# Kernel optimization log

Hardware: AMD Instinct MI355X
Metric: run time of the kernel (lower is better)

The kernel has to match this reference:

```python
import jax, jax.numpy as jnp
import numpy as np

B, S, H = 8, 2048, 1024

def setup_inputs() -> dict:
    key = jax.random.key(0)
    ks = jax.random.split(key, 7)
    scale = 1.0 / np.sqrt(H)
    return {
        "x": jax.random.normal(ks[0], (B, S, H), dtype=jnp.float32),
        "Wq": jax.random.uniform(ks[1], (H, H), jnp.float32, -scale, scale),
        "bq": jax.random.uniform(ks[2], (H,), jnp.float32, -scale, scale),
        "Wk": jax.random.uniform(ks[3], (H, H), jnp.float32, -scale, scale),
        "bk": jax.random.uniform(ks[4], (H,), jnp.float32, -scale, scale),
        "Wv": jax.random.uniform(ks[5], (H, H), jnp.float32, -scale, scale),
        "bv": jax.random.uniform(ks[6], (H,), jnp.float32, -scale, scale),
    }

def reference(x, Wq, bq, Wk, bk, Wv, bv):
    # nn.Linear: x @ W.T + b  (dropout_rate=0.0 -> identity)
    q = jnp.einsum("bsh,oh->bso", x, Wq) + bq
    k = jnp.einsum("bsh,oh->bso", x, Wk) + bk
    v = jnp.einsum("bsh,oh->bso", x, Wv) + bv
    # NOTE: original module applies NO 1/sqrt(d) scaling
    scores = jnp.einsum("bqh,bkh->bqk", q, k)  # [B,S,S]
    probs = jax.nn.softmax(scores, axis=-1)
    context = jnp.einsum("bqk,bkh->bqh", probs, v)  # [B,S,H]
    return context
```

## Files before the change

### kernel.cpp

```cpp
#include <hip/hip_runtime.h>
#include <stdint.h>

typedef unsigned short UST;
typedef __attribute__((ext_vector_type(8))) short    bf16x8;
typedef __attribute__((ext_vector_type(4))) float    f32x4;
typedef __attribute__((ext_vector_type(4))) float    float4_t;
typedef __attribute__((ext_vector_type(4))) UST      ushort4_t;
typedef __attribute__((ext_vector_type(8))) UST      ushort8_t;

__device__ __forceinline__ UST f2bf(float f) {
    union { float f; uint32_t u; } c; c.f = f;
    uint32_t u = c.u;
    u = (u + 0x7FFFu + ((u >> 16) & 1u)) >> 16;
    return (UST)u;
}
__device__ __forceinline__ float bf2f(UST h) {
    union { uint32_t u; float f; } c; c.u = ((uint32_t)h) << 16;
    return c.f;
}

__device__ __forceinline__ void async_copy16(const void* g, void* l) {
    __builtin_amdgcn_global_load_lds(
        (const __attribute__((address_space(1))) uint32_t*)g,
        (__attribute__((address_space(3))) uint32_t*)l, 16, 0, 0);
}

__device__ __forceinline__ void xcd_remap(int& bx, int& by, int& bz) {
    const int gx = (int)gridDim.x, gy = (int)gridDim.y, gz = (int)gridDim.z;
    const int nwg = gx * gy * gz;
    if (nwg & 7) return;
    int flat = ((int)blockIdx.z * gy + (int)blockIdx.y) * gx + (int)blockIdx.x;
    const int q = nwg >> 3;
    int s = (flat & 7) * q + (flat >> 3);
    bx = s % gx; s /= gx;
    by = s % gy;
    bz = s / gy;
}

__global__ void split_kernel(const float* __restrict__ in, UST* __restrict__ hi,
                             UST* __restrict__ lo, int n4) {
    int i = blockIdx.x * blockDim.x + threadIdx.x;
    int stride = gridDim.x * blockDim.x;
    for (; i < n4; i += stride) {
        float4_t v = *(const float4_t*)(in + (size_t)i * 4);
        ushort4_t h, l;
#pragma unroll
        for (int j = 0; j < 4; j++) {
            float f = v[j];
            UST hh = f2bf(f);
            h[j] = hh;
            l[j] = f2bf(f - bf2f(hh));
        }
        *(ushort4_t*)(hi + (size_t)i * 4) = h;
        *(ushort4_t*)(lo + (size_t)i * 4) = l;
    }
}

__global__ void cvt_hi_kernel(const float* __restrict__ in, UST* __restrict__ hi, int n4) {
    int i = blockIdx.x * blockDim.x + threadIdx.x;
    int stride = gridDim.x * blockDim.x;
    for (; i < n4; i += stride) {
        float4_t v = *(const float4_t*)(in + (size_t)i * 4);
        ushort4_t h;
#pragma unroll
        for (int j = 0; j < 4; j++) h[j] = f2bf(v[j]);
        *(ushort4_t*)(hi + (size_t)i * 4) = h;
    }
}

template <int OUT_MODE, bool HAS_BIAS>
__global__ __launch_bounds__(512, 2)
void gemm3_256(const UST* __restrict__ Ah, const UST* __restrict__ Al,
               const UST* __restrict__ Bh, const UST* __restrict__ Bl,
               const float* __restrict__ bias,
               void* __restrict__ C0, void* __restrict__ C1,
               int K, int ldc,
               long long sA, long long sB, long long sC) {
    constexpr int TILE = 8192;
    constexpr int HALF = 4 * TILE;
    __shared__ UST lds[2 * HALF];

    int bx = (int)blockIdx.x, by = (int)blockIdx.y, bz = (int)blockIdx.z;
    xcd_remap(bx, by, bz);
    const int brow = by * 256;
    const int bcol = bx * 256;

    const int t = threadIdx.x;
    const int wave = t >> 6, lane = t & 63;
    const int wr = (wave >> 2) * 128;
    const int wc = (wave & 3) * 64;
    const int lr = lane & 15, lg = lane >> 4;

    const int srow0 = t >> 2;
    const int scol_sw = (((t & 3) ^ ((srow0 >> 1) & 3))) * 8;

    int offA[8], offB[4];
#pragma unroll
    for (int m = 0; m < 8; m++) {
        int r = wr + m * 16 + lr;
        offA[m] = r * 32 + ((lg ^ ((r >> 1) & 3)) << 3);
    }
#pragma unroll
    for (int n = 0; n < 4; n++) {
        int r = wc + n * 16 + lr;
        offB[n] = r * 32 + ((lg ^ ((r >> 1) & 3)) << 3);
    }

    f32x4 acc[8][4];
#pragma unroll
    for (int m = 0; m < 8; m++)
#pragma unroll
        for (int n = 0; n < 4; n++) acc[m][n] = (f32x4){0.f, 0.f, 0.f, 0.f};

    const UST* pAh = Ah + (long long)bz * sA;
    const UST* pAl = Al + (long long)bz * sA;
    const UST* pBh = Bh + (long long)bz * sB;
    const UST* pBl = Bl + (long long)bz * sB;

    {
        const UST* gAh = pAh + (size_t)(brow + srow0) * (size_t)K + scol_sw;
        async_copy16(gAh, lds + t * 8);
        async_copy16(gAh + (size_t)128 * K, lds + 4096 + t * 8);
        const UST* gAl = pAl + (size_t)(brow + srow0) * (size_t)K + scol_sw;
        async_copy16(gAl, lds + TILE + t * 8);
        async_copy16(gAl + (size_t)128 * K, lds + TILE + 4096 + t * 8);
        const UST* gBh = pBh + (size_t)(bcol + srow0) * (size_t)K + scol_sw;
        async_copy16(gBh, lds + 2 * TILE + t * 8);
        async_copy16(gBh + (size_t)128 * K, lds + 2 * TILE + 4096 + t * 8);
        const UST* gBl = pBl + (size_t)(bcol + srow0) * (size_t)K + scol_sw;
        async_copy16(gBl, lds + 3 * TILE + t * 8);
        async_copy16(gBl + (size_t)128 * K, lds + 3 * TILE + 4096 + t * 8);
        asm volatile("s_waitcnt vmcnt(0)" ::: "memory");
        __builtin_amdgcn_s_barrier();
    }

    int cur = 0;
    const int nt = K / 32;
    for (int it = 0; it < nt; ++it) {
        UST* buf  = lds + cur * HALF;
        UST* nbuf = lds + (cur ^ 1) * HALF;
        const bool pf = (it + 1 < nt);
        const int k1 = (it + 1) * 32;

        bf16x8 ah_[4], al_[4], bh_[4], bl_[4];

#pragma unroll
        for (int m = 0; m < 4; m++) ah_[m] = *(const bf16x8*)(buf + offA[m]);
#pragma unroll
        for (int n = 0; n < 4; n++) bh_[n] = *(const bf16x8*)(buf + 2 * TILE + offB[n]);
        if (pf) {
            const UST* gAh = pAh + (size_t)(brow + srow0) * (size_t)K + k1 + scol_sw;
            async_copy16(gAh, nbuf + t * 8);
            async_copy16(gAh + (size_t)128 * K, nbuf + 4096 + t * 8);
            const UST* gAl = pAl + (size_t)(brow + srow0) * (size_t)K + k1 + scol_sw;
            async_copy16(gAl, nbuf + TILE + t * 8);
            async_copy16(gAl + (size_t)128 * K, nbuf + TILE + 4096 + t * 8);
        }
        __builtin_amdgcn_s_barrier();
        asm volatile("s_waitcnt lgkmcnt(0)" ::: "memory");
        __builtin_amdgcn_sched_barrier(0);
        __builtin_amdgcn_s_setprio(1);
#pragma unroll
        for (int m = 0; m < 4; m++)
#pragma unroll
            for (int n = 0; n < 4; n++)
                acc[m][n] = __builtin_amdgcn_mfma_f32_16x16x32_bf16(ah_[m], bh_[n], acc[m][n], 0, 0, 0);
        __builtin_amdgcn_s_setprio(0);
        __builtin_amdgcn_s_barrier();

#pragma unroll
        for (int m = 0; m < 4; m++) al_[m] = *(const bf16x8*)(buf + TILE + offA[m]);
        if (pf) {
            const UST* gBh = pBh + (size_t)(bcol + srow0) * (size_t)K + k1 + scol_sw;
            async_copy16(gBh, nbuf + 2 * TILE + t * 8);
            async_copy16(gBh + (size_t)128 * K, nbuf + 2 * TILE + 4096 + t * 8);
            const UST* gBl = pBl + (size_t)(bcol + srow0) * (size_t)K + k1 + scol_sw;
            async_copy16(gBl, nbuf + 3 * TILE + t * 8);
            async_copy16(gBl + (size_t)128 * K, nbuf + 3 * TILE + 4096 + t * 8);
        }
        __builtin_amdgcn_s_barrier();
        asm volatile("s_waitcnt lgkmcnt(0)" ::: "memory");
        __builtin_amdgcn_sched_barrier(0);
        __builtin_amdgcn_s_setprio(1);
#pragma unroll
        for (int m = 0; m < 4; m++)
#pragma unroll
            for (int n = 0; n < 4; n++)
                acc[m][n] = __builtin_amdgcn_mfma_f32_16x16x32_bf16(al_[m], bh_[n], acc[m][n], 0, 0, 0);
        __builtin_amdgcn_s_setprio(0);
        __builtin_amdgcn_s_barrier();

#pragma unroll
        for (int n = 0; n < 4; n++) bl_[n] = *(const bf16x8*)(buf + 3 * TILE + offB[n]);
        __builtin_amdgcn_s_barrier();
        asm volatile("s_waitcnt lgkmcnt(0)" ::: "memory");
        __builtin_amdgcn_sched_barrier(0);
        __builtin_amdgcn_s_setprio(1);
#pragma unroll
        for (int m = 0; m < 4; m++)
#pragma unroll
            for (int n = 0; n < 4; n++)
                acc[m][n] = __builtin_amdgcn_mfma_f32_16x16x32_bf16(ah_[m], bl_[n], acc[m][n], 0, 0, 0);
        __builtin_amdgcn_s_setprio(0);
        __builtin_amdgcn_s_barrier();

#pragma unroll
        for (int m = 0; m < 4; m++) ah_[m] = *(const bf16x8*)(buf + offA[m + 4]);
        __builtin_amdgcn_s_barrier();
        asm volatile("s_waitcnt lgkmcnt(0)" ::: "memory");
        __builtin_amdgcn_sched_barrier(0);
        __builtin_amdgcn_s_setprio(1);
#pragma unroll
        for (int m = 0; m < 4; m++)
#pragma unroll
            for (int n = 0; n < 4; n++)
                acc[m + 4][n] = __builtin_amdgcn_mfma_f32_16x16x32_bf16(ah_[m], bh_[n], acc[m + 4][n], 0, 0, 0);
        __builtin_amdgcn_s_setprio(0);
        __builtin_amdgcn_s_barrier();

#pragma unroll
        for (int m = 0; m < 4; m++) al_[m] = *(const bf16x8*)(buf + TILE + offA[m + 4]);
        __builtin_amdgcn_s_barrier();
        asm volatile("s_waitcnt lgkmcnt(0)" ::: "memory");
        __builtin_amdgcn_sched_barrier(0);
        __builtin_amdgcn_s_setprio(1);
#pragma unroll
        for (int m = 0; m < 4; m++)
#pragma unroll
            for (int n = 0; n < 4; n++)
                acc[m + 4][n] = __builtin_amdgcn_mfma_f32_16x16x32_bf16(al_[m], bh_[n], acc[m + 4][n], 0, 0, 0);
        __builtin_amdgcn_s_setprio(0);
        __builtin_amdgcn_s_barrier();

        asm volatile("s_waitcnt vmcnt(0)" ::: "memory");
        __builtin_amdgcn_sched_barrier(0);
        __builtin_amdgcn_s_barrier();
        __builtin_amdgcn_s_setprio(1);
#pragma unroll
        for (int m = 0; m < 4; m++)
#pragma unroll
            for (int n = 0; n < 4; n++)
                acc[m + 4][n] = __builtin_amdgcn_mfma_f32_16x16x32_bf16(ah_[m], bl_[n], acc[m + 4][n], 0, 0, 0);
        __builtin_amdgcn_s_setprio(0);
        __builtin_amdgcn_s_barrier();

        cur ^= 1;
    }

    float bvv[4];
#pragma unroll
    for (int n = 0; n < 4; n++)
        bvv[n] = HAS_BIAS ? bias[bcol + wc + n * 16 + lr] : 0.0f;

#pragma unroll
    for (int m = 0; m < 8; m++) {
        const int row0 = brow + wr + m * 16 + lg * 4;
#pragma unroll
        for (int n = 0; n < 4; n++) {
            const int col = bcol + wc + n * 16 + lr;
            if constexpr (OUT_MODE == 0) {
                float* C = (float*)C0 + (long long)bz * sC;
#pragma unroll
                for (int j = 0; j < 4; j++)
                    C[(size_t)(row0 + j) * ldc + col] = acc[m][n][j] + bvv[n];
            } else {
                UST* Hh = (UST*)C0 + (long long)bz * sC;
                UST* Ll = (UST*)C1 + (long long)bz * sC;
#pragma unroll
                for (int j = 0; j < 4; j++) {
                    float v = acc[m][n][j] + bvv[n];
                    UST h = f2bf(v);
                    Hh[(size_t)(row0 + j) * ldc + col] = h;
                    Ll[(size_t)(row0 + j) * ldc + col] = f2bf(v - bf2f(h));
                }
            }
        }
    }
}

template <int OUT_MODE, bool HAS_BIAS>
__global__ __launch_bounds__(256, 2)
void gemm_bt(const UST* __restrict__ Aptr, const UST* __restrict__ Bptr,
             const float* __restrict__ bias,
             void* __restrict__ C0,
             int K, int ldc,
             long long sA, long long sB, long long sC) {
    constexpr int HALF = 8192;
    __shared__ UST lds[16384];

    int bx = (int)blockIdx.x, by = (int)blockIdx.y, bz = (int)blockIdx.z;
    xcd_remap(bx, by, bz);
    const int brow = by * 128;
    const int bcol = bx * 128;

    const int t = threadIdx.x;
    const int wave = t >> 6, lane = t & 63;
    const int wr = (wave >> 1) * 64, wc = (wave & 1) * 64;
    const int lr = lane & 15, lg = lane >> 4;

    const int srow = t >> 2;
    const int scol_sw = (((t & 3) ^ ((srow >> 1) & 3))) * 8;

    int offA[4], offB[4];
#pragma unroll
    for (int m = 0; m < 4; m++) {
        int r = wr + m * 16 + lr;
        offA[m] = r * 32 + ((lg ^ ((r >> 1) & 3)) << 3);
    }
#pragma unroll
    for (int n = 0; n < 4; n++) {
        int r = wc + n * 16 + lr;
        offB[n] = r * 32 + ((lg ^ ((r >> 1) & 3)) << 3);
    }

    f32x4 acc[4][4];
#pragma unroll
    for (int m = 0; m < 4; m++)
#pragma unroll
        for (int n = 0; n < 4; n++) acc[m][n] = (f32x4){0.f, 0.f, 0.f, 0.f};

    const UST* Ah = Aptr + (long long)bz * sA;
    const UST* Bh = Bptr + (long long)bz * sB;

    auto stage = [&](UST* dst, int k0) {
        const UST* gA = Ah + (size_t)(brow + srow) * (size_t)K + k0 + scol_sw;
        async_copy16(gA, dst + t * 8);
        async_copy16(gA + (size_t)64 * K, dst + 2048 + t * 8);
        const UST* gB = Bh + (size_t)(bcol + srow) * (size_t)K + k0 + scol_sw;
        async_copy16(gB, dst + 4096 + t * 8);
        async_copy16(gB + (size_t)64 * K, dst + 6144 + t * 8);
    };

    stage(lds, 0);
    int cur = 0;
    const int nt = K / 32;
    for (int it = 0; it < nt; ++it) {
        UST* buf = lds + cur * HALF;
        __builtin_amdgcn_s_barrier();
        if (it + 1 < nt) {
            stage(lds + (cur ^ 1) * HALF, (it + 1) * 32);
            asm volatile("s_waitcnt vmcnt(4)" ::: "memory");
        } else {
            asm volatile("s_waitcnt vmcnt(0)" ::: "memory");
        }
        __builtin_amdgcn_sched_barrier(0);
        __builtin_amdgcn_s_barrier();

        bf16x8 ah[4], bh[4];
#pragma unroll
        for (int m = 0; m < 4; m++) ah[m] = *(const bf16x8*)(buf + offA[m]);
#pragma unroll
        for (int n = 0; n < 4; n++) bh[n] = *(const bf16x8*)(buf + 4096 + offB[n]);

        __builtin_amdgcn_s_setprio(1);
#pragma unroll
        for (int m = 0; m < 4; m++)
#pragma unroll
            for (int n = 0; n < 4; n++)
                acc[m][n] = __builtin_amdgcn_mfma_f32_16x16x32_bf16(ah[m], bh[n], acc[m][n], 0, 0, 0);
        __builtin_amdgcn_s_setprio(0);
        cur ^= 1;
    }

    float bvv[4];
#pragma unroll
    for (int n = 0; n < 4; n++)
        bvv[n] = HAS_BIAS ? bias[bcol + wc + n * 16 + lr] : 0.0f;

    if constexpr (OUT_MODE == 2) {
        __syncthreads();
#pragma unroll
        for (int m = 0; m < 4; m++) {
            const int r0 = wr + m * 16 + lg * 4;
#pragma unroll
            for (int n = 0; n < 4; n++) {
                const int c = wc + n * 16 + lr;
                ushort4_t pk;
#pragma unroll
                for (int j = 0; j < 4; j++) pk[j] = f2bf(acc[m][n][j] + bvv[n]);
                *(ushort4_t*)(lds + c * 128 + r0) = pk;
            }
        }
        __syncthreads();
        UST* V = (UST*)C0 + (long long)bz * sC;
        const int hl = t >> 1, soff = (t & 1) * 64;
        const UST* src = lds + hl * 128 + soff;
        UST* dst = V + (size_t)(bcol + hl) * ldc + brow + soff;
#pragma unroll
        for (int i = 0; i < 8; i++)
            *(ushort8_t*)(dst + i * 8) = *(const ushort8_t*)(src + i * 8);
        return;
    }

#pragma unroll
    for (int m = 0; m < 4; m++) {
        const int row0 = brow + wr + m * 16 + lg * 4;
#pragma unroll
        for (int n = 0; n < 4; n++) {
            const int col = bcol + wc + n * 16 + lr;
            float* C = (float*)C0 + (long long)bz * sC;
#pragma unroll
            for (int j = 0; j < 4; j++)
                C[(size_t)(row0 + j) * ldc + col] = acc[m][n][j] + bvv[n];
        }
    }
}

__global__ __launch_bounds__(256)
void softmax_bf16(const float* __restrict__ S, UST* __restrict__ P) {
    const size_t row = blockIdx.x;
    const float* s = S + row * 2048;
    const int t = threadIdx.x;
    const int wave = t >> 6, lane = t & 63;

    float4_t v0 = *(const float4_t*)(s + t * 8);
    float4_t v1 = *(const float4_t*)(s + t * 8 + 4);
    float vv[8];
#pragma unroll
    for (int j = 0; j < 4; j++) { vv[j] = v0[j]; vv[4 + j] = v1[j]; }

    float m = vv[0];
#pragma unroll
    for (int j = 1; j < 8; j++) m = fmaxf(m, vv[j]);
#pragma unroll
    for (int off = 32; off; off >>= 1) m = fmaxf(m, __shfl_xor(m, off));

    __shared__ float red[16];
    if (lane == 0) red[wave] = m;
    __syncthreads();
    m = fmaxf(fmaxf(red[0], red[1]), fmaxf(red[2], red[3]));

    float e[8];
    float sum = 0.f;
#pragma unroll
    for (int j = 0; j < 8; j++) { e[j] = __expf(vv[j] - m); sum += e[j]; }
#pragma unroll
    for (int off = 32; off; off >>= 1) sum += __shfl_xor(sum, off);
    if (lane == 0) red[8 + wave] = sum;
    __syncthreads();
    sum = red[8] + red[9] + red[10] + red[11];

    float inv = 1.0f / sum;
    ushort8_t pk;
#pragma unroll
    for (int j = 0; j < 8; j++) pk[j] = f2bf(e[j] * inv);
    *(ushort8_t*)(P + row * 2048 + t * 8) = pk;
}

extern "C" void kernel_launch(void* const* d_in, const int* in_sizes, int n_in,
                              void* d_out, int out_size, void* d_ws, size_t ws_size,
                              hipStream_t stream) {
    (void)in_sizes; (void)n_in; (void)out_size;
    const float* x  = (const float*)d_in[0];
    const float* Wq = (const float*)d_in[1];
    const float* bq = (const float*)d_in[2];
    const float* Wk = (const float*)d_in[3];
    const float* bk = (const float*)d_in[4];
    const float* Wv = (const float*)d_in[5];
    const float* bv = (const float*)d_in[6];
    float* out = (float*)d_out;

    const int B = 8, S = 2048, H = 1024;
    const size_t BSH = (size_t)B * S * H;
    const long long sXH = (long long)S * H;

    char* p = (char*)d_ws;
    UST* qh = (UST*)p; p += BSH * 2;
    UST* ql = (UST*)p; p += BSH * 2;
    UST* kh = (UST*)p; p += BSH * 2;
    UST* kl = (UST*)p; p += BSH * 2;
    UST* vt = (UST*)p; p += BSH * 2;

    const size_t fixed = (size_t)(p - (char*)d_ws);
    const size_t perB = (size_t)S * S * 6;
    const size_t avail = ws_size > fixed ? ws_size - fixed : 0;

    const size_t HH = (size_t)H * H;

    char* q = p;
    UST* xh  = (UST*)q; q += BSH * 2;
    UST* xl  = (UST*)q; q += BSH * 2;
    UST* wqh = (UST*)q; q += HH * 2;
    UST* wql = (UST*)q; q += HH * 2;
    UST* wkh = (UST*)q; q += HH * 2;
    UST* wkl = (UST*)q; q += HH * 2;
    UST* wvh = (UST*)q; q += HH * 2;

    dim3 blk(256);
    dim3 blk512(512);

    split_kernel<<<2048, blk, 0, stream>>>(x, xh, xl, (int)(BSH / 4));
    split_kernel<<<256, blk, 0, stream>>>(Wq, wqh, wql, (int)(HH / 4));
    split_kernel<<<256, blk, 0, stream>>>(Wk, wkh, wkl, (int)(HH / 4));
    cvt_hi_kernel<<<256, blk, 0, stream>>>(Wv, wvh, (int)(HH / 4));

    dim3 gproj3(H / 256, S / 256, B);
    gemm3_256<1, true><<<gproj3, blk512, 0, stream>>>(
        xh, xl, wqh, wql, bq, qh, ql, H, H, sXH, 0, sXH);
    gemm3_256<1, true><<<gproj3, blk512, 0, stream>>>(
        xh, xl, wkh, wkl, bk, kh, kl, H, H, sXH, 0, sXH);
    dim3 gprojv(H / 128, S / 128, B);
    gemm_bt<2, true><<<gprojv, blk, 0, stream>>>(
        xh, wvh, bv, vt, H, S, sXH, 0, (long long)H * S);

    int g = (int)(avail / perB);
    if (g >= 1) {
        if (g > 8) g = 8;
        while (8 % g) g--;
        float* scores = (float*)p;
        UST* probs = (UST*)(p + (size_t)g * S * S * 4);

        for (int b0 = 0; b0 < B; b0 += g) {
            const size_t ob = (size_t)b0 * S * H;
            dim3 gsc(S / 256, S / 256, g);
            gemm3_256<0, false><<<gsc, blk512, 0, stream>>>(
                qh + ob, ql + ob, kh + ob, kl + ob, nullptr,
                scores, nullptr, H, S, sXH, sXH, (long long)S * S);

            softmax_bf16<<<g * S, blk, 0, stream>>>(scores, probs);

            dim3 gpv(H / 128, S / 128, g);
            gemm_bt<0, false><<<gpv, blk, 0, stream>>>(
                probs, vt + (size_t)b0 * H * S, nullptr,
                out + ob, S, H,
                (long long)S * S, (long long)H * S, sXH);
        }
    } else {
        int rows = (int)(avail / ((size_t)S * 6 * 256)) * 256;
        if (rows < 256) rows = 256;
        if (rows > S) rows = S;
        float* scores = (float*)p;
        UST* probs = (UST*)(p + (size_t)rows * S * 4);

        for (int b = 0; b < B; b++) {
            for (int r0 = 0; r0 < S; r0 += rows) {
                int rc = S - r0 < rows ? S - r0 : rows;
                const size_t ob = (size_t)b * S * H + (size_t)r0 * H;
                dim3 gsc(S / 256, rc / 256, 1);
                gemm3_256<0, false><<<gsc, blk512, 0, stream>>>(
                    qh + ob, ql + ob, kh + (size_t)b * S * H, kl + (size_t)b * S * H,
                    nullptr, scores, nullptr, H, S, 0, 0, 0);

                softmax_bf16<<<rc, blk, 0, stream>>>(scores, probs);

                dim3 gpv(H / 128, rc / 128, 1);
                gemm_bt<0, false><<<gpv, blk, 0, stream>>>(
                    probs, vt + (size_t)b * H * S, nullptr,
                    out + ob, S, H, 0, 0, 0);
            }
        }
    }
}
```

Measured before the change: 556.7 us.

## Spread tile prefetches across MFMA phases with partial vmcnt waits and fewer barriers

```diff
diff --git a/kernel.cpp b/kernel.cpp
--- a/kernel.cpp
+++ b/kernel.cpp
@@ -117,22 +117,20 @@
     const UST* pBh = Bh + (long long)bz * sB;
     const UST* pBl = Bl + (long long)bz * sB;
 
-    {
-        const UST* gAh = pAh + (size_t)(brow + srow0) * (size_t)K + scol_sw;
-        async_copy16(gAh, lds + t * 8);
-        async_copy16(gAh + (size_t)128 * K, lds + 4096 + t * 8);
-        const UST* gAl = pAl + (size_t)(brow + srow0) * (size_t)K + scol_sw;
-        async_copy16(gAl, lds + TILE + t * 8);
-        async_copy16(gAl + (size_t)128 * K, lds + TILE + 4096 + t * 8);
-        const UST* gBh = pBh + (size_t)(bcol + srow0) * (size_t)K + scol_sw;
-        async_copy16(gBh, lds + 2 * TILE + t * 8);
-        async_copy16(gBh + (size_t)128 * K, lds + 2 * TILE + 4096 + t * 8);
-        const UST* gBl = pBl + (size_t)(bcol + srow0) * (size_t)K + scol_sw;
-        async_copy16(gBl, lds + 3 * TILE + t * 8);
-        async_copy16(gBl + (size_t)128 * K, lds + 3 * TILE + 4096 + t * 8);
-        asm volatile("s_waitcnt vmcnt(0)" ::: "memory");
-        __builtin_amdgcn_s_barrier();
-    }
+    auto stage2 = [&](const UST* g, UST* dst) {
+        async_copy16(g, dst + t * 8);
+        async_copy16(g + (size_t)128 * K, dst + 4096 + t * 8);
+    };
+    const size_t arow = (size_t)(brow + srow0) * (size_t)K + scol_sw;
+    const size_t brow_ = (size_t)(bcol + srow0) * (size_t)K + scol_sw;
+
+    stage2(pAh + arow, lds);
+    stage2(pAl + arow, lds + TILE);
+    stage2(pBh + brow_, lds + 2 * TILE);
+    stage2(pBl + brow_, lds + 3 * TILE);
+    asm volatile("s_waitcnt vmcnt(2)" ::: "memory");
+    __builtin_amdgcn_sched_barrier(0);
+    __builtin_amdgcn_s_barrier();
 
     int cur = 0;
     const int nt = K / 32;
@@ -148,14 +146,7 @@
         for (int m = 0; m < 4; m++) ah_[m] = *(const bf16x8*)(buf + offA[m]);
 #pragma unroll
         for (int n = 0; n < 4; n++) bh_[n] = *(const bf16x8*)(buf + 2 * TILE + offB[n]);
-        if (pf) {
-            const UST* gAh = pAh + (size_t)(brow + srow0) * (size_t)K + k1 + scol_sw;
-            async_copy16(gAh, nbuf + t * 8);
-            async_copy16(gAh + (size_t)128 * K, nbuf + 4096 + t * 8);
-            const UST* gAl = pAl + (size_t)(brow + srow0) * (size_t)K + k1 + scol_sw;
-            async_copy16(gAl, nbuf + TILE + t * 8);
-            async_copy16(gAl + (size_t)128 * K, nbuf + TILE + 4096 + t * 8);
-        }
+        if (pf) stage2(pAh + arow + k1, nbuf);
         __builtin_amdgcn_s_barrier();
         asm volatile("s_waitcnt lgkmcnt(0)" ::: "memory");
         __builtin_amdgcn_sched_barrier(0);
@@ -166,17 +157,14 @@
             for (int n = 0; n < 4; n++)
                 acc[m][n] = __builtin_amdgcn_mfma_f32_16x16x32_bf16(ah_[m], bh_[n], acc[m][n], 0, 0, 0);
         __builtin_amdgcn_s_setprio(0);
-        __builtin_amdgcn_s_barrier();
 
 #pragma unroll
         for (int m = 0; m < 4; m++) al_[m] = *(const bf16x8*)(buf + TILE + offA[m]);
         if (pf) {
-            const UST* gBh = pBh + (size_t)(bcol + srow0) * (size_t)K + k1 + scol_sw;
-            async_copy16(gBh, nbuf + 2 * TILE + t * 8);
-            async_copy16(gBh + (size_t)128 * K, nbuf + 2 * TILE + 4096 + t * 8);
-            const UST* gBl = pBl + (size_t)(bcol + srow0) * (size_t)K + k1 + scol_sw;
-            async_copy16(gBl, nbuf + 3 * TILE + t * 8);
-            async_copy16(gBl + (size_t)128 * K, nbuf + 3 * TILE + 4096 + t * 8);
+            stage2(pAl + arow + k1, nbuf + TILE);
+            asm volatile("s_waitcnt vmcnt(4)" ::: "memory");
+        } else {
+            asm volatile("s_waitcnt vmcnt(0)" ::: "memory");
         }
         __builtin_amdgcn_s_barrier();
         asm volatile("s_waitcnt lgkmcnt(0)" ::: "memory");
@@ -188,10 +176,10 @@
             for (int n = 0; n < 4; n++)
                 acc[m][n] = __builtin_amdgcn_mfma_f32_16x16x32_bf16(al_[m], bh_[n], acc[m][n], 0, 0, 0);
         __builtin_amdgcn_s_setprio(0);
-        __builtin_amdgcn_s_barrier();
 
 #pragma unroll
         for (int n = 0; n < 4; n++) bl_[n] = *(const bf16x8*)(buf + 3 * TILE + offB[n]);
+        if (pf) stage2(pBh + brow_ + k1, nbuf + 2 * TILE);
         __builtin_amdgcn_s_barrier();
         asm volatile("s_waitcnt lgkmcnt(0)" ::: "memory");
         __builtin_amdgcn_sched_barrier(0);
@@ -202,10 +190,10 @@
             for (int n = 0; n < 4; n++)
                 acc[m][n] = __builtin_amdgcn_mfma_f32_16x16x32_bf16(ah_[m], bl_[n], acc[m][n], 0, 0, 0);
         __builtin_amdgcn_s_setprio(0);
-        __builtin_amdgcn_s_barrier();
 
 #pragma unroll
         for (int m = 0; m < 4; m++) ah_[m] = *(const bf16x8*)(buf + offA[m + 4]);
+        if (pf) stage2(pBl + brow_ + k1, nbuf + 3 * TILE);
         __builtin_amdgcn_s_barrier();
         asm volatile("s_waitcnt lgkmcnt(0)" ::: "memory");
         __builtin_amdgcn_sched_barrier(0);
@@ -216,7 +204,6 @@
             for (int n = 0; n < 4; n++)
                 acc[m + 4][n] = __builtin_amdgcn_mfma_f32_16x16x32_bf16(ah_[m], bh_[n], acc[m + 4][n], 0, 0, 0);
         __builtin_amdgcn_s_setprio(0);
-        __builtin_amdgcn_s_barrier();
 
 #pragma unroll
         for (int m = 0; m < 4; m++) al_[m] = *(const bf16x8*)(buf + TILE + offA[m + 4]);
@@ -230,9 +217,10 @@
             for (int n = 0; n < 4; n++)
                 acc[m + 4][n] = __builtin_amdgcn_mfma_f32_16x16x32_bf16(al_[m], bh_[n], acc[m + 4][n], 0, 0, 0);
         __builtin_amdgcn_s_setprio(0);
-        __builtin_amdgcn_s_barrier();
-
-        asm volatile("s_waitcnt vmcnt(0)" ::: "memory");
+
+        if (pf) {
+            asm volatile("s_waitcnt vmcnt(2)" ::: "memory");
+        }
         __builtin_amdgcn_sched_barrier(0);
         __builtin_amdgcn_s_barrier();
         __builtin_amdgcn_s_setprio(1);
@@ -242,7 +230,6 @@
             for (int n = 0; n < 4; n++)
                 acc[m + 4][n] = __builtin_amdgcn_mfma_f32_16x16x32_bf16(ah_[m], bl_[n], acc[m + 4][n], 0, 0, 0);
         __builtin_amdgcn_s_setprio(0);
-        __builtin_amdgcn_s_barrier();
 
         cur ^= 1;
     }
```

After: 536.5 us. 1.04x faster.
